# Kernel tuning notes

Hardware: AMD Instinct MI355X
Metric: run time of the kernel (lower is better)

## Reference

```python
import jax, jax.numpy as jnp
import numpy as np

B, T, C = 4, 2048, 1024
H, HS = 16, 64


def setup_inputs() -> dict:
    key = jax.random.key(0)
    ks = jax.random.split(key, 5)
    scale = (H * C) ** (-0.5)
    x = jax.random.normal(ks[0], (B, T, C), dtype=jnp.float32)
    Wk = jax.random.normal(ks[1], (H, C, HS), dtype=jnp.float32) * scale
    Wq = jax.random.normal(ks[2], (H, C, HS), dtype=jnp.float32) * scale
    Wv = jax.random.normal(ks[3], (H, C, HS), dtype=jnp.float32) * scale
    proj_w = jax.random.normal(ks[4], (C, C), dtype=jnp.float32) / C ** 0.5
    proj_b = jnp.zeros((C,), dtype=jnp.float32)
    return {"x": x, "Wk": Wk, "Wq": Wq, "Wv": Wv, "proj_w": proj_w, "proj_b": proj_b}


def reference(x, Wk, Wq, Wv, proj_w, proj_b):
    b, t, c = x.shape
    # per-head projections: (B,T,C) x (H,C,D) -> (B,H,T,D)
    q = jnp.einsum('btc,hcd->bhtd', x, Wq)
    k = jnp.einsum('btc,hcd->bhtd', x, Wk)
    v = jnp.einsum('btc,hcd->bhtd', x, Wv)
    # NOTE: original module does not scale by 1/sqrt(head_size)
    wei = jnp.einsum('bhtd,bhsd->bhts', q, k)  # (B,H,T,T)
    causal = jnp.tril(jnp.ones((t, t), dtype=bool))
    wei = jnp.where(causal, wei, -jnp.inf)
    wei = jax.nn.softmax(wei, axis=-1)
    out = jnp.einsum('bhts,bhsd->bhtd', wei, v)
    out = out.transpose(0, 2, 1, 3).reshape(b, t, c)  # concat heads
    return out @ proj_w + proj_b
```

## Files before the change

kernel.cpp:

```cpp
#include <hip/hip_runtime.h>

typedef unsigned short u16;
typedef u16 u16x4 __attribute__((ext_vector_type(4)));
typedef u16 u16x8 __attribute__((ext_vector_type(8)));
typedef unsigned uint2v __attribute__((ext_vector_type(2)));
typedef unsigned uint4v __attribute__((ext_vector_type(4)));
typedef __bf16 bf16x2 __attribute__((ext_vector_type(2)));
typedef __bf16 bf16x8 __attribute__((ext_vector_type(8)));
typedef float f32x4 __attribute__((ext_vector_type(4)));

#define DEV static __device__ __forceinline__

DEV u16 f2bf(float f) {
  union { float f; unsigned u; } v; v.f = f;
  return (u16)((v.u + 0x7FFFu + ((v.u >> 16) & 1u)) >> 16);
}

DEV void async16(const void* g, void* l) {
  __builtin_amdgcn_global_load_lds((const __attribute__((address_space(1))) void*)g,
                                   (__attribute__((address_space(3))) void*)l, 16, 0, 0);
}

DEV f32x4 mfma16(bf16x8 a, bf16x8 b, f32x4 c) {
  return __builtin_amdgcn_mfma_f32_16x16x32_bf16(a, b, c, 0, 0, 0);
}

DEV float exp2fast(float x) { return __builtin_amdgcn_exp2f(x); }

__global__ __launch_bounds__(256) void k_prep(const float* __restrict__ x,
                                              const float* __restrict__ Wk,
                                              const float* __restrict__ Wq,
                                              const float* __restrict__ Wv,
                                              const float* __restrict__ pw,
                                              u16* __restrict__ xb,
                                              u16* __restrict__ wT,
                                              u16* __restrict__ pwT) {
  __shared__ float t[64 * 72];
  const int bid = blockIdx.x, tid = threadIdx.x;
  if (bid < 8192) {
    int i = bid * 1024 + tid * 4;
    float4 v = *(const float4*)(x + i);
    u16x4 o = { f2bf(v.x), f2bf(v.y), f2bf(v.z), f2bf(v.w) };
    *(u16x4*)(xb + i) = o;
    return;
  }
  const int role = bid - 8192;
  const float* src;
  u16* dst;
  int rows, cols, bx, by, bz;
  float scale;
  if (role < 768) {
    const int w = role >> 8, rem = role & 255;
    src = (w == 0) ? Wq : ((w == 1) ? Wk : Wv);
    dst = wT + (size_t)w * 1024 * 1024;
    scale = (w == 0) ? 1.44269504088896340736f : 1.0f;
    rows = 1024; cols = 64; bx = 0; by = rem >> 4; bz = rem & 15;
  } else {
    const int p = role - 768;
    src = pw; dst = pwT; scale = 1.0f;
    rows = 1024; cols = 1024; bx = p & 15; by = p >> 4; bz = 0;
  }
  src += (size_t)bz * rows * cols;
  dst += (size_t)bz * rows * cols;
  const int c0 = bx * 64, r0 = by * 64;
  const int rr = tid >> 2, cb = (tid & 3) * 16;
  const float* s = src + (size_t)(r0 + rr) * cols + c0 + cb;
  float4 v0 = *(const float4*)(s + 0);
  float4 v1 = *(const float4*)(s + 4);
  float4 v2 = *(const float4*)(s + 8);
  float4 v3 = *(const float4*)(s + 12);
  *(float4*)(t + rr * 72 + cb + 0)  = v0;
  *(float4*)(t + rr * 72 + cb + 4)  = v1;
  *(float4*)(t + rr * 72 + cb + 8)  = v2;
  *(float4*)(t + rr * 72 + cb + 12) = v3;
  __syncthreads();
  const int dd = tid >> 2, eb = (tid & 3) * 16;
  u16x8 o0, o1;
#pragma unroll
  for (int e = 0; e < 8; ++e) o0[e] = f2bf(t[(eb + e) * 72 + dd] * scale);
#pragma unroll
  for (int e = 0; e < 8; ++e) o1[e] = f2bf(t[(eb + 8 + e) * 72 + dd] * scale);
  u16* dp = dst + (size_t)(c0 + dd) * rows + r0 + eb;
  *(u16x8*)dp = o0;
  *(u16x8*)(dp + 8) = o1;
}

template <int MODE>
__global__ __launch_bounds__(512, 2) void k_gemm(const u16* __restrict__ A,
                                                 const u16* __restrict__ Bt,
                                                 u16* __restrict__ qd,
                                                 u16* __restrict__ kd,
                                                 u16* __restrict__ vd,
                                                 float* __restrict__ out,
                                                 const float* __restrict__ bias) {
  constexpr int BN   = (MODE == 0) ? 256 : 128;
  constexpr int AI   = (MODE == 0) ? 8 : 4;
  constexpr int AJ   = 4;
  constexpr int WN   = (MODE == 0) ? 4 : 2;
  constexpr int GB   = BN / 64;
  constexpr int GXC  = (MODE == 0) ? 12 : 8;
  constexpr int STEPU = (256 + BN) * 64;
  __shared__ u16 lds[2 * STEPU];

  const int tid = threadIdx.x;
  const int w = tid >> 6, lane = tid & 63;
  const int quad = lane >> 4, l15 = lane & 15;
  const int wm = w / WN, wn = w % WN;

  constexpr int NWG = GXC * 32;
  int lin = (int)blockIdx.y * GXC + (int)blockIdx.x;
  lin = (lin & 7) * (NWG >> 3) + (lin >> 3);
  const size_t mb = (size_t)(lin / GXC);
  const int nb = lin % GXC;

  const int lr = lane >> 3;
  const int lc = ((lane & 7) ^ lr) << 3;
  const u16* ga0 = A  + (mb * 256 + (size_t)(w * 8 + lr)) * 1024 + lc;
  const u16* gb0 = Bt + ((size_t)nb * BN + (size_t)(w * 8 + lr)) * 1024 + lc;

  const int swz0 = ((0 + quad) ^ (l15 & 7)) << 3;
  const int swz1 = ((4 + quad) ^ (l15 & 7)) << 3;

  f32x4 acc[AI][AJ] = {};

  auto STAGE = [&](int buf, int s) {
    u16* sb = lds + buf * STEPU + w * 512;
    const int ko = s * 64;
#pragma unroll
    for (int g = 0; g < 4; ++g)
      async16(ga0 + (size_t)g * 65536 + ko, sb + g * 4096);
#pragma unroll
    for (int g = 0; g < GB; ++g)
      async16(gb0 + (size_t)g * 65536 + ko, sb + 16384 + g * 4096);
  };

  STAGE(0, 0);
  __syncthreads();

  for (int s = 0; s < 16; ++s) {
    const int buf = s & 1;
    if (s < 15) STAGE(buf ^ 1, s + 1);
    const u16* Ab = lds + buf * STEPU;
    const u16* Bb = Ab + 16384;

#pragma unroll
    for (int c = 0; c < 2; ++c) {
      const int swz = c ? swz1 : swz0;
      bf16x8 af[AI], bf[AJ];
#pragma unroll
      for (int i = 0; i < AI; ++i)
        af[i] = *(const bf16x8*)(Ab + (wm * (AI * 16) + i * 16 + l15) * 64 + swz);
#pragma unroll
      for (int j = 0; j < AJ; ++j)
        bf[j] = *(const bf16x8*)(Bb + (wn * (AJ * 16) + j * 16 + l15) * 64 + swz);
      __builtin_amdgcn_s_setprio(1);
#pragma unroll
      for (int i = 0; i < AI; ++i)
#pragma unroll
        for (int j = 0; j < AJ; ++j) acc[i][j] = mfma16(af[i], bf[j], acc[i][j]);
      __builtin_amdgcn_s_setprio(0);
    }
    __syncthreads();
  }

  const size_t m0 = mb * 256 + wm * (AI * 16);
  const int n0 = nb * BN + wn * (AJ * 16);
  if (MODE == 0) {
#pragma unroll
    for (int j = 0; j < AJ; ++j) {
      const int n = n0 + j * 16 + l15;
      const int p = n >> 10, hh = (n >> 6) & 15, d = n & 63;
      if (p == 2) {
#pragma unroll
        for (int i = 0; i < AI; ++i) {
          const size_t m = m0 + i * 16 + quad * 4;
          const size_t bb = m >> 11, tt = m & 2047;
          u16x4 pk = { f2bf(acc[i][j][0]), f2bf(acc[i][j][1]),
                       f2bf(acc[i][j][2]), f2bf(acc[i][j][3]) };
          *(u16x4*)(vd + ((bb * 16 + hh) * 64 + d) * 2048 + tt) = pk;
        }
      } else {
        u16* dst = (p == 0) ? qd : kd;
#pragma unroll
        for (int i = 0; i < AI; ++i)
#pragma unroll
          for (int r = 0; r < 4; ++r) {
            const size_t m = m0 + i * 16 + quad * 4 + r;
            const size_t bb = m >> 11, tt = m & 2047;
            dst[((bb * 16 + hh) * 2048 + tt) * 64 + d] = f2bf(acc[i][j][r]);
          }
      }
    }
  } else {
#pragma unroll
    for (int j = 0; j < AJ; ++j) {
      const int n = n0 + j * 16 + l15;
      const float bv = bias[n];
#pragma unroll
      for (int i = 0; i < AI; ++i)
#pragma unroll
        for (int r = 0; r < 4; ++r) {
          const size_t m = m0 + i * 16 + quad * 4 + r;
          out[m * 1024 + n] = acc[i][j][r] + bv;
        }
    }
  }
}

__global__ __launch_bounds__(256) void k_attn(const u16* __restrict__ Qg,
                                              const u16* __restrict__ Kg,
                                              const u16* __restrict__ Vtg,
                                              u16* __restrict__ Og) {
  __shared__ u16 Kbuf[2 * 4096];
  __shared__ u16 Vbuf[2 * 4096];
  const int tid = threadIdx.x;
  const int wave = tid >> 6, lane = tid & 63;
  const int quad = lane >> 4, l15 = lane & 15;
  const int quad4 = quad * 4, quad8 = quad * 8;
  const int bh = blockIdx.x;
  const int qb = 15 - (int)blockIdx.y;
  const u16* kg = Kg + (size_t)bh * 2048 * 64;
  const u16* vg = Vtg + (size_t)bh * 64 * 2048;
  const int b = bh >> 4, h = bh & 15;

  const int lrow = lane >> 3;
  const int lchunk = ((lane & 7) ^ lrow) << 3;
  const u16* kst = kg + (size_t)(wave * 16 + lrow) * 64 + lchunk;
  const u16* vst = vg + (size_t)(wave * 16 + lrow) * 2048 + lchunk;
  u16* kdst0 = Kbuf + wave * 1024;
  u16* vdst0 = Vbuf + wave * 1024;

  const int rowoff = l15 * 64;
  const int swz0 = ((0 + quad) ^ (l15 & 7)) << 3;
  const int swz1 = ((4 + quad) ^ (l15 & 7)) << 3;

  const int qlo = qb * 128 + wave * 32;
  const int ntw = 2 * qb + 1 + (wave >> 1);
  const int ntb = 2 * qb + 2;
  const u16* qg = Qg + ((size_t)bh * 2048 + (size_t)qb * 128) * 64;

  bf16x8 qf[2][2];
#pragma unroll
  for (int i = 0; i < 2; ++i)
#pragma unroll
    for (int c = 0; c < 2; ++c)
      qf[i][c] = *(const bf16x8*)(qg + (size_t)(wave * 32 + i * 16 + l15) * 64 +
                                  c * 32 + quad8);

  f32x4 oacc[2][4] = {};
  f32x4 lacc[2] = {};
  const f32x4 fzero = {};
  const u16x8 onesu = {0x3F80, 0x3F80, 0x3F80, 0x3F80,
                       0x3F80, 0x3F80, 0x3F80, 0x3F80};
  const bf16x8 onesf = __builtin_bit_cast(bf16x8, onesu);

  async16(kst, kdst0);
  async16(kst + 512, kdst0 + 512);
  async16(vst, vdst0);
  async16(vst + 16384, vdst0 + 512);

  for (int it = 0; it < ntb; ++it) {
    __syncthreads();

    if (it + 1 < ntb) {
      const int buf = (it + 1) & 1;
      const size_t s0n = (size_t)(it + 1) * 64;
      async16(kst + s0n * 64,       kdst0 + buf * 4096);
      async16(kst + s0n * 64 + 512, kdst0 + buf * 4096 + 512);
      async16(vst + s0n,            vdst0 + buf * 4096);
      async16(vst + s0n + 16384,    vdst0 + buf * 4096 + 512);
    }

    if (it < ntw) {
      const int s0 = it * 64;
      const u16* Kb = Kbuf + (it & 1) * 4096;
      const u16* Vb = Vbuf + (it & 1) * 4096;

      f32x4 sacc[4][2];
      __builtin_amdgcn_s_setprio(1);
#pragma unroll
      for (int j = 0; j < 4; ++j) {
        bf16x8 kf0 = *(const bf16x8*)(Kb + j * 1024 + rowoff + swz0);
        bf16x8 kf1 = *(const bf16x8*)(Kb + j * 1024 + rowoff + swz1);
        sacc[j][0] = mfma16(kf0, qf[0][0], fzero);
        sacc[j][0] = mfma16(kf1, qf[0][1], sacc[j][0]);
        sacc[j][1] = mfma16(kf0, qf[1][0], fzero);
        sacc[j][1] = mfma16(kf1, qf[1][1], sacc[j][1]);
      }
      __builtin_amdgcn_s_setprio(0);

#pragma unroll
      for (int j = 0; j < 4; ++j)
#pragma unroll
        for (int i = 0; i < 2; ++i)
#pragma unroll
          for (int r = 0; r < 4; ++r)
            sacc[j][i][r] = exp2fast(sacc[j][i][r]);

      if (it == ntw - 1) {
#pragma unroll
        for (int j = 0; j < 4; ++j)
#pragma unroll
        for (int i = 0; i < 2; ++i)
#pragma unroll
          for (int r = 0; r < 4; ++r)
            if (s0 + j * 16 + quad4 + r > qlo + i * 16 + l15) sacc[j][i][r] = 0.f;
      }

      bf16x8 pa[2][2];
#pragma unroll
      for (int i = 0; i < 2; ++i) {
        unsigned P[8];
#pragma unroll
        for (int j = 0; j < 4; ++j) {
          bf16x2 lo = { (__bf16)sacc[j][i][0], (__bf16)sacc[j][i][1] };
          bf16x2 hi = { (__bf16)sacc[j][i][2], (__bf16)sacc[j][i][3] };
          P[j * 2 + 0] = __builtin_bit_cast(unsigned, lo);
          P[j * 2 + 1] = __builtin_bit_cast(unsigned, hi);
        }
        unsigned wd[8];
#pragma unroll
        for (int g = 0; g < 4; ++g) {
          const int x = (g & 2) * 2 + (g & 1);
          uint2v t = __builtin_amdgcn_permlane32_swap(P[x], P[x + 2], false, false);
          uint2v u = __builtin_amdgcn_permlane16_swap(t.x, t.y, false, false);
          wd[x] = u.x;
          wd[x + 2] = u.y;
        }
        uint4v lo4 = { wd[0], wd[1], wd[2], wd[3] };
        uint4v hi4 = { wd[4], wd[5], wd[6], wd[7] };
        pa[i][0] = __builtin_bit_cast(bf16x8, lo4);
        pa[i][1] = __builtin_bit_cast(bf16x8, hi4);
      }

      __builtin_amdgcn_s_setprio(1);
#pragma unroll
      for (int n = 0; n < 4; ++n) {
        bf16x8 vf0 = *(const bf16x8*)(Vb + n * 1024 + rowoff + swz0);
        bf16x8 vf1 = *(const bf16x8*)(Vb + n * 1024 + rowoff + swz1);
        oacc[0][n] = mfma16(pa[0][0], vf0, oacc[0][n]);
        oacc[0][n] = mfma16(pa[0][1], vf1, oacc[0][n]);
        oacc[1][n] = mfma16(pa[1][0], vf0, oacc[1][n]);
        oacc[1][n] = mfma16(pa[1][1], vf1, oacc[1][n]);
      }
      lacc[0] = mfma16(pa[0][0], onesf, lacc[0]);
      lacc[0] = mfma16(pa[0][1], onesf, lacc[0]);
      lacc[1] = mfma16(pa[1][0], onesf, lacc[1]);
      lacc[1] = mfma16(pa[1][1], onesf, lacc[1]);
      __builtin_amdgcn_s_setprio(0);
    }
  }

#pragma unroll
  for (int i = 0; i < 2; ++i)
#pragma unroll
    for (int r = 0; r < 4; ++r) {
      const float inv = 1.0f / lacc[i][r];
      const size_t t = (size_t)qb * 128 + wave * 32 + i * 16 + quad4 + r;
#pragma unroll
      for (int n = 0; n < 4; ++n)
        Og[((size_t)b * 2048 + t) * 1024 + h * 64 + n * 16 + l15] =
            f2bf(oacc[i][n][r] * inv);
    }
}

extern "C" void kernel_launch(void* const* d_in, const int* in_sizes, int n_in,
                              void* d_out, int out_size, void* d_ws, size_t ws_size,
                              hipStream_t stream) {
  const float* x  = (const float*)d_in[0];
  const float* Wk = (const float*)d_in[1];
  const float* Wq = (const float*)d_in[2];
  const float* Wv = (const float*)d_in[3];
  const float* pw = (const float*)d_in[4];
  const float* pb = (const float*)d_in[5];
  float* out = (float*)d_out;
  char* ws = (char*)d_ws;

  u16* xb  = (u16*)(ws + 0);
  u16* wT  = (u16*)(ws + 16777216);
  u16* pwT = (u16*)(ws + 23068672);
  u16* q   = (u16*)(ws + 25165824);
  u16* kb  = (u16*)(ws + 41943040);
  u16* vt  = (u16*)(ws + 58720256);
  u16* att = (u16*)(ws + 0);

  k_prep<<<9216, 256, 0, stream>>>(x, Wk, Wq, Wv, pw, xb, wT, pwT);
  k_gemm<0><<<dim3(12, 32), 512, 0, stream>>>(xb, wT, q, kb, vt, nullptr, nullptr);
  k_attn<<<dim3(64, 16), 256, 0, stream>>>(q, kb, vt, att);
  k_gemm<1><<<dim3(8, 32), 512, 0, stream>>>(att, pwT, nullptr, nullptr, nullptr, out, pb);
}
```

Baseline: 241.7 us.

## Restructure GEMM pipelines with split-phase barriers and a triple-buffered projection ring

The QKV GEMM tile changes from 256x256 to 256x192 with a 16-column grid, giving 512 workgroups instead of 384 for better CU fill. Both GEMMs now use an explicit schedule in which LDS fragment reads, async global-to-LDS loads and MFMA phases are separated by raw s_barrier and sched_barrier. The output-projection GEMM gets a 3-slot LDS ring with prefetch two steps ahead and partial vmcnt waits, to hide load latency better. In exchange there are more barriers per k-step and more LDS for the projection kernel, which may reduce occupancy. Correctness now rests on hand-placed waitcnt values.

```diff
diff --git a/kernel.cpp b/kernel.cpp
--- a/kernel.cpp
+++ b/kernel.cpp
@@ -26,6 +26,9 @@
 }
 
 DEV float exp2fast(float x) { return __builtin_amdgcn_exp2f(x); }
+
+#define BARRIER() asm volatile("s_barrier" ::: "memory")
+#define SB0() __builtin_amdgcn_sched_barrier(0)
 
 __global__ __launch_bounds__(256) void k_prep(const float* __restrict__ x,
                                               const float* __restrict__ Wk,
@@ -93,19 +96,20 @@
                                                  u16* __restrict__ vd,
                                                  float* __restrict__ out,
                                                  const float* __restrict__ bias) {
-  constexpr int BN   = (MODE == 0) ? 256 : 128;
+  constexpr int BN   = (MODE == 0) ? 192 : 128;
   constexpr int AI   = (MODE == 0) ? 8 : 4;
-  constexpr int AJ   = 4;
-  constexpr int WN   = (MODE == 0) ? 4 : 2;
+  constexpr int AJ   = (MODE == 0) ? 3 : 4;
   constexpr int GB   = BN / 64;
-  constexpr int GXC  = (MODE == 0) ? 12 : 8;
-  constexpr int STEPU = (256 + BN) * 64;
-  __shared__ u16 lds[2 * STEPU];
+  constexpr int GXC  = (MODE == 0) ? 16 : 8;
+  constexpr int SLOT = (256 + BN) * 64;
+  constexpr int RING = (MODE == 0) ? 2 : 3;
+  __shared__ u16 lds[RING * SLOT];
 
   const int tid = threadIdx.x;
   const int w = tid >> 6, lane = tid & 63;
   const int quad = lane >> 4, l15 = lane & 15;
-  const int wm = w / WN, wn = w % WN;
+  const int wm = (MODE == 0) ? (w >> 2) : (w >> 1);
+  const int wn = (MODE == 0) ? (w & 3) : (w & 1);
 
   constexpr int NWG = GXC * 32;
   int lin = (int)blockIdx.y * GXC + (int)blockIdx.x;
@@ -123,44 +127,136 @@
 
   f32x4 acc[AI][AJ] = {};
 
-  auto STAGE = [&](int buf, int s) {
-    u16* sb = lds + buf * STEPU + w * 512;
-    const int ko = s * 64;
-#pragma unroll
-    for (int g = 0; g < 4; ++g)
-      async16(ga0 + (size_t)g * 65536 + ko, sb + g * 4096);
-#pragma unroll
-    for (int g = 0; g < GB; ++g)
-      async16(gb0 + (size_t)g * 65536 + ko, sb + 16384 + g * 4096);
-  };
-
-  STAGE(0, 0);
-  __syncthreads();
-
-  for (int s = 0; s < 16; ++s) {
-    const int buf = s & 1;
-    if (s < 15) STAGE(buf ^ 1, s + 1);
-    const u16* Ab = lds + buf * STEPU;
-    const u16* Bb = Ab + 16384;
-
-#pragma unroll
-    for (int c = 0; c < 2; ++c) {
-      const int swz = c ? swz1 : swz0;
-      bf16x8 af[AI], bf[AJ];
-#pragma unroll
-      for (int i = 0; i < AI; ++i)
-        af[i] = *(const bf16x8*)(Ab + (wm * (AI * 16) + i * 16 + l15) * 64 + swz);
+  if constexpr (MODE == 0) {
+    {
+      u16* sb = lds + w * 512;
+#pragma unroll
+      for (int g = 0; g < 4; ++g) async16(ga0 + (size_t)g * 65536, sb + g * 4096);
+#pragma unroll
+      for (int g = 0; g < GB; ++g) async16(gb0 + (size_t)g * 65536, sb + 16384 + g * 4096);
+    }
+    asm volatile("s_waitcnt vmcnt(0)" ::: "memory");
+    BARRIER(); SB0();
+
+    for (int s = 0; s < 16; ++s) {
+      const u16* Ab = lds + (s & 1) * SLOT;
+      const u16* Bb = Ab + 16384;
+      u16* nsb = lds + ((s + 1) & 1) * SLOT + w * 512;
+      const int ko = (s + 1) * 64;
+
+      bf16x8 a0[AI], b0[AJ];
+#pragma unroll
+      for (int i = 0; i < AI; ++i)
+        a0[i] = *(const bf16x8*)(Ab + (wm * (AI * 16) + i * 16 + l15) * 64 + swz0);
 #pragma unroll
       for (int j = 0; j < AJ; ++j)
-        bf[j] = *(const bf16x8*)(Bb + (wn * (AJ * 16) + j * 16 + l15) * 64 + swz);
-      __builtin_amdgcn_s_setprio(1);
-#pragma unroll
-      for (int i = 0; i < AI; ++i)
-#pragma unroll
-        for (int j = 0; j < AJ; ++j) acc[i][j] = mfma16(af[i], bf[j], acc[i][j]);
-      __builtin_amdgcn_s_setprio(0);
-    }
-    __syncthreads();
+        b0[j] = *(const bf16x8*)(Bb + (wn * (AJ * 16) + j * 16 + l15) * 64 + swz0);
+      if (s < 15) {
+#pragma unroll
+        for (int g = 0; g < 4; ++g)
+          async16(ga0 + (size_t)g * 65536 + ko, nsb + g * 4096);
+      }
+      SB0(); BARRIER(); SB0();
+      __builtin_amdgcn_s_setprio(1);
+#pragma unroll
+      for (int i = 0; i < AI; ++i)
+#pragma unroll
+        for (int j = 0; j < AJ; ++j) acc[i][j] = mfma16(a0[i], b0[j], acc[i][j]);
+      __builtin_amdgcn_s_setprio(0);
+      SB0(); BARRIER(); SB0();
+
+      bf16x8 a1[AI], b1[AJ];
+#pragma unroll
+      for (int i = 0; i < AI; ++i)
+        a1[i] = *(const bf16x8*)(Ab + (wm * (AI * 16) + i * 16 + l15) * 64 + swz1);
+#pragma unroll
+      for (int j = 0; j < AJ; ++j)
+        b1[j] = *(const bf16x8*)(Bb + (wn * (AJ * 16) + j * 16 + l15) * 64 + swz1);
+      if (s < 15) {
+#pragma unroll
+        for (int g = 0; g < GB; ++g)
+          async16(gb0 + (size_t)g * 65536 + ko, nsb + 16384 + g * 4096);
+      }
+      SB0(); BARRIER(); SB0();
+      __builtin_amdgcn_s_setprio(1);
+#pragma unroll
+      for (int i = 0; i < AI; ++i)
+#pragma unroll
+        for (int j = 0; j < AJ; ++j) acc[i][j] = mfma16(a1[i], b1[j], acc[i][j]);
+      __builtin_amdgcn_s_setprio(0);
+      SB0();
+      if (s < 15) {
+        asm volatile("s_waitcnt vmcnt(0) lgkmcnt(0)" ::: "memory");
+        BARRIER(); SB0();
+      }
+    }
+  } else {
+    auto STAGE = [&](int buf, int s) {
+      u16* sb = lds + buf * SLOT + w * 512;
+      const int ko = s * 64;
+#pragma unroll
+      for (int g = 0; g < 4; ++g)
+        async16(ga0 + (size_t)g * 65536 + ko, sb + g * 4096);
+#pragma unroll
+      for (int g = 0; g < GB; ++g)
+        async16(gb0 + (size_t)g * 65536 + ko, sb + 16384 + g * 4096);
+    };
+    STAGE(0, 0);
+    STAGE(1, 1);
+    asm volatile("s_waitcnt vmcnt(6)" ::: "memory");
+    BARRIER(); SB0();
+
+    for (int s = 0; s < 16; ++s) {
+      const u16* Ab = lds + (s % 3) * SLOT;
+      const u16* Bb = Ab + 16384;
+
+      bf16x8 a0[AI], b0[AJ];
+#pragma unroll
+      for (int i = 0; i < AI; ++i)
+        a0[i] = *(const bf16x8*)(Ab + (wm * (AI * 16) + i * 16 + l15) * 64 + swz0);
+#pragma unroll
+      for (int j = 0; j < AJ; ++j)
+        b0[j] = *(const bf16x8*)(Bb + (wn * (AJ * 16) + j * 16 + l15) * 64 + swz0);
+      if (s < 14) {
+        u16* d = lds + ((s + 2) % 3) * SLOT + w * 512;
+        async16(ga0 + 0 * 65536 + (s + 2) * 64, d + 0 * 4096);
+        async16(ga0 + 1 * 65536 + (s + 2) * 64, d + 1 * 4096);
+        async16(ga0 + 2 * 65536 + (s + 2) * 64, d + 2 * 4096);
+      }
+      SB0(); BARRIER(); SB0();
+      __builtin_amdgcn_s_setprio(1);
+#pragma unroll
+      for (int i = 0; i < AI; ++i)
+#pragma unroll
+        for (int j = 0; j < AJ; ++j) acc[i][j] = mfma16(a0[i], b0[j], acc[i][j]);
+      __builtin_amdgcn_s_setprio(0);
+      SB0(); BARRIER(); SB0();
+
+      bf16x8 a1[AI], b1[AJ];
+#pragma unroll
+      for (int i = 0; i < AI; ++i)
+        a1[i] = *(const bf16x8*)(Ab + (wm * (AI * 16) + i * 16 + l15) * 64 + swz1);
+#pragma unroll
+      for (int j = 0; j < AJ; ++j)
+        b1[j] = *(const bf16x8*)(Bb + (wn * (AJ * 16) + j * 16 + l15) * 64 + swz1);
+      if (s < 14) {
+        u16* d = lds + ((s + 2) % 3) * SLOT + w * 512;
+        async16(ga0 + 3 * 65536 + (s + 2) * 64, d + 3 * 4096);
+        async16(gb0 + 0 * 65536 + (s + 2) * 64, d + 16384 + 0 * 4096);
+        async16(gb0 + 1 * 65536 + (s + 2) * 64, d + 16384 + 4096);
+      }
+      SB0(); BARRIER(); SB0();
+      __builtin_amdgcn_s_setprio(1);
+#pragma unroll
+      for (int i = 0; i < AI; ++i)
+#pragma unroll
+        for (int j = 0; j < AJ; ++j) acc[i][j] = mfma16(a1[i], b1[j], acc[i][j]);
+      __builtin_amdgcn_s_setprio(0);
+      SB0();
+      if (s < 14)       { asm volatile("s_waitcnt vmcnt(6)" ::: "memory"); }
+      else if (s == 14) { asm volatile("s_waitcnt vmcnt(0)" ::: "memory"); }
+      if (s < 15) { BARRIER(); SB0(); }
+    }
   }
 
   const size_t m0 = mb * 256 + wm * (AI * 16);
@@ -385,7 +481,7 @@
   u16* att = (u16*)(ws + 0);
 
   k_prep<<<9216, 256, 0, stream>>>(x, Wk, Wq, Wv, pw, xb, wT, pwT);
-  k_gemm<0><<<dim3(12, 32), 512, 0, stream>>>(xb, wT, q, kb, vt, nullptr, nullptr);
+  k_gemm<0><<<dim3(16, 32), 512, 0, stream>>>(xb, wT, q, kb, vt, nullptr, nullptr);
   k_attn<<<dim3(64, 16), 256, 0, stream>>>(q, kb, vt, att);
   k_gemm<1><<<dim3(8, 32), 512, 0, stream>>>(att, pwT, nullptr, nullptr, nullptr, out, pb);
 }
```

Measured after the change: 231.4 us. 4.3% less time.
